# Performance work log

Measured on AMD Instinct MI355X. Metric: run time of the kernel, lower is better.

The kernel has to match this reference:

```python
import jax, jax.numpy as jnp
import numpy as np


def _conv1x1(W, x):
    # W: (out_c, in_c) from a 1x1 Conv2d (bias=False); x: (b, in_c, h, w)
    return jnp.einsum('oc,bchw->bohw', W, x)


def setup_inputs() -> dict:
    key = jax.random.key(0)
    ks = jax.random.split(key, 7)
    b, c, h, w = 4, 256, 64, 64
    inter = c // 2
    out_c = 256
    s = 0.02
    return {
        'A': jax.random.normal(ks[0], (b, c, h, w), dtype=jnp.float32),
        'B': jax.random.normal(ks[1], (b, c, h, w), dtype=jnp.float32),
        'W_phi': jax.random.normal(ks[2], (inter, c), dtype=jnp.float32) * s,
        'W_theta': jax.random.normal(ks[3], (inter, c), dtype=jnp.float32) * s,
        'W_g': jax.random.normal(ks[4], (inter, 2 * c), dtype=jnp.float32) * s,
        'W_AB': jax.random.normal(ks[5], (out_c, 2 * c), dtype=jnp.float32) * s,
        'W_mask': jax.random.normal(ks[6], (out_c, inter), dtype=jnp.float32) * s,
    }


def reference(A, B, W_phi, W_theta, W_g, W_AB, W_mask):
    b, c, h, w = A.shape
    inter = c // 2
    AB = jnp.concatenate([A, B], axis=1)  # (b, 2c, h, w)
    # NOTE: original torch code views (b, c/2, h*w) as (b, c, h*w/2) -> seq len N = h*w/2
    x_phi = _conv1x1(W_phi, A).reshape(b, c, -1)                       # (b, c, N)
    x_theta = _conv1x1(W_theta, B).reshape(b, c, -1).transpose(0, 2, 1)  # (b, N, c)
    x_g = _conv1x1(W_g, AB).reshape(b, c, -1).transpose(0, 2, 1)       # (b, N, c)
    scores = jnp.einsum('bnc,bcm->bnm', x_theta, x_phi)                # (b, N, N)
    attn = jax.nn.softmax(scores, axis=1)  # softmax over dim=1 as in torch code
    y = jnp.einsum('bnm,bmc->bnc', attn, x_g)                          # (b, N, c)
    y = y.transpose(0, 2, 1).reshape(b, inter, h, w)
    out = _conv1x1(W_mask, y) + _conv1x1(W_AB, AB)
    return out
```

## Files before the change

### kernel.cpp

```cpp
#include <hip/hip_runtime.h>
#include <hip/hip_bf16.h>

#define B_    4
#define C_    256
#define HW    4096
#define N_    2048
#define BSTR  524288

typedef unsigned short u16;
using f32x4 = __attribute__((ext_vector_type(4))) float;
using u32x4 = __attribute__((ext_vector_type(4))) unsigned int;

__device__ __forceinline__ float bf2f(u16 u) {
    return __uint_as_float(((unsigned)u) << 16);
}
__device__ __forceinline__ u16 f2bf(float f) {
    unsigned x = __float_as_uint(f);
    x += 0x7fff + ((x >> 16) & 1);
    return (u16)(x >> 16);
}

__device__ __forceinline__ void mfma_bf16(f32x4& acc, u32x4 a, u32x4 b) {
    asm volatile("v_mfma_f32_16x16x32_bf16 %0, %1, %2, %0"
                 : "+v"(acc) : "v"(a), "v"(b));
}
__device__ __forceinline__ void mfma_bf16_vsrc(f32x4& acc, u32x4 a, u32x4 b) {
    asm volatile("s_nop 1\n\tv_mfma_f32_16x16x32_bf16 %0, %1, %2, %0"
                 : "+v"(acc) : "v"(a), "v"(b));
}
__device__ __forceinline__ void mfma_fence(f32x4& x) {
    asm volatile("s_nop 7\n\ts_nop 7" : "+v"(x));
}

__global__ __launch_bounds__(256) void prep_w(
    const float* __restrict__ Wphi, const float* __restrict__ Wtheta,
    const float* __restrict__ Wg, const float* __restrict__ Wab,
    u16* __restrict__ Wt)
{
    const int row = blockIdx.x;
    const int t   = threadIdx.x;
    #pragma unroll
    for (int i = 0; i < 2; ++i) {
        const int col = i * 256 + t;
        float v;
        if (row < 128)      v = (col < 256)  ? Wphi[row * 256 + col] : 0.f;
        else if (row < 256) v = (col >= 256) ? Wtheta[(row - 128) * 256 + (col - 256)] : 0.f;
        else if (row < 384) v = Wg[(row - 256) * 512 + col];
        else                v = Wab[(row - 384) * 512 + col];
        Wt[row * 512 + col] = f2bf(v);
    }
}

__global__ __launch_bounds__(256) void prep_abt(
    const float* __restrict__ A, const float* __restrict__ Bx,
    u16* __restrict__ ABt)
{
    __shared__ u16 L[64][528];
    const int t = threadIdx.x, pb = blockIdx.x, b = blockIdx.y;
    const int p0 = pb * 64;
    const int pl = t & 63, cg = t >> 6;
    const float* Ab = A  + (size_t)b * C_ * HW;
    const float* Bb = Bx + (size_t)b * C_ * HW;

    for (int i = 0; i < 64; ++i) {
        const int c = cg + i * 4;
        L[pl][c]       = f2bf(Ab[c * HW + p0 + pl]);
        L[pl][256 + c] = f2bf(Bb[c * HW + p0 + pl]);
    }
    __syncthreads();
    u16* dst = ABt + ((size_t)b * 4096 + p0) * 512;
    #pragma unroll
    for (int i = 0; i < 16; ++i) {
        const int idx = i * 256 + t;
        const int row = idx >> 6, ch = idx & 63;
        *(uint4*)&dst[row * 512 + ch * 8] = *(const uint4*)&L[row][ch * 8];
    }
}

__global__ __launch_bounds__(256) void conv_gemm(
    const u16* __restrict__ Wt, const u16* __restrict__ ABt,
    u16* __restrict__ phit, u16* __restrict__ thetat,
    u16* __restrict__ g, float* __restrict__ out)
{
    __shared__ __align__(16) u16 shW[64 * 128];
    __shared__ __align__(16) u16 shAB[64 * 128];
    const int t = threadIdx.x, pb = blockIdx.x, nb = blockIdx.y, b = blockIdx.z;
    const int lane = t & 63, w = t >> 6, lo = lane & 15, hi = lane >> 4;
    const u16* Wb = Wt + nb * 64 * 512;
    const u16* Ab = ABt + ((size_t)b * 4096 + pb * 64) * 512;

    f32x4 acc[4];
    #pragma unroll
    for (int ot = 0; ot < 4; ++ot) acc[ot] = (f32x4){0.f, 0.f, 0.f, 0.f};

    for (int ks = 0; ks < 4; ++ks) {
        __syncthreads();
        #pragma unroll
        for (int i = 0; i < 4; ++i) {
            const int q = i * 256 + t;
            const int row = q >> 4, c16 = (q & 15) * 8;
            const int sw = (row & 7) << 3;
            *(uint4*)&shW[row * 128 + (c16 ^ sw)]  = *(const uint4*)&Wb[row * 512 + ks * 128 + c16];
            *(uint4*)&shAB[row * 128 + (c16 ^ sw)] = *(const uint4*)&Ab[row * 512 + ks * 128 + c16];
        }
        __syncthreads();
        u32x4 bfr[4];
        {
            const int row = w * 16 + lo, sw = (row & 7) << 3;
            #pragma unroll
            for (int kf = 0; kf < 4; ++kf)
                bfr[kf] = *(const u32x4*)&shAB[row * 128 + ((kf * 32 + hi * 8) ^ sw)];
        }
        #pragma unroll
        for (int ot = 0; ot < 4; ++ot) {
            const int row = ot * 16 + lo, sw = (row & 7) << 3;
            #pragma unroll
            for (int kf = 0; kf < 4; ++kf) {
                const u32x4 a = *(const u32x4*)&shW[row * 128 + ((kf * 32 + hi * 8) ^ sw)];
                mfma_bf16(acc[ot], a, bfr[kf]);
            }
        }
    }

    const int p_global = pb * 64 + w * 16 + lo;
    const int m = p_global & 2047, h = p_global >> 11;
    #pragma unroll
    for (int ot = 0; ot < 4; ++ot) {
        mfma_fence(acc[ot]);
        const int ob = nb * 64 + ot * 16 + hi * 4;
        if (nb < 2) {
            ushort4 v;
            v.x = f2bf(acc[ot][0]); v.y = f2bf(acc[ot][1]);
            v.z = f2bf(acc[ot][2]); v.w = f2bf(acc[ot][3]);
            *(ushort4*)&phit[(size_t)b * BSTR + m * 256 + h * 128 + ob] = v;
        } else if (nb < 4) {
            ushort4 v;
            v.x = f2bf(acc[ot][0]); v.y = f2bf(acc[ot][1]);
            v.z = f2bf(acc[ot][2]); v.w = f2bf(acc[ot][3]);
            *(ushort4*)&thetat[(size_t)b * BSTR + m * 256 + h * 128 + (ob - 128)] = v;
        } else if (nb < 6) {
            #pragma unroll
            for (int q = 0; q < 4; ++q)
                g[(size_t)b * BSTR + (ob - 256 + q) * HW + p_global] = f2bf(acc[ot][q]);
        } else {
            #pragma unroll
            for (int q = 0; q < 4; ++q)
                out[(size_t)b * C_ * HW + (size_t)(ob - 384 + q) * HW + p_global] = acc[ot][q];
        }
    }
}

__global__ __launch_bounds__(256) void passA_mfma(
    const u16* __restrict__ phit, const u16* __restrict__ thetat,
    float* __restrict__ rs)
{
    __shared__ __align__(16) u16 shP[64 * 256];
    __shared__ __align__(16) u16 shT[64 * 256];
    const int t = threadIdx.x, b = blockIdx.z, nq = blockIdx.y, mb = blockIdx.x;
    const u16* Pb = phit   + b * BSTR + mb * 64 * 256;
    const u16* Tb = thetat + b * BSTR + nq * 512 * 256;

    #pragma unroll
    for (int i = 0; i < 8; ++i) {
        const int q = i * 256 + t;
        const int row = q >> 5, c16 = (q & 31) * 8;
        const uint4 v = *(const uint4*)&Pb[row * 256 + c16];
        *(uint4*)&shP[row * 256 + (c16 ^ ((row & 7) << 3))] = v;
    }
    __syncthreads();

    const int lane = t & 63, w = t >> 6, lo = lane & 15, hi = lane >> 4;
    u32x4 afr[8];
    {
        const int row = w * 16 + lo;
        #pragma unroll
        for (int kb = 0; kb < 8; ++kb)
            afr[kb] = *(const u32x4*)&shP[row * 256 + ((kb * 32 + hi * 8) ^ ((row & 7) << 3))];
    }

    float rsacc[4] = {0.f, 0.f, 0.f, 0.f};
    for (int nt = 0; nt < 8; ++nt) {
        __syncthreads();
        #pragma unroll
        for (int i = 0; i < 8; ++i) {
            const int q = i * 256 + t;
            const int row = q >> 5, c16 = (q & 31) * 8;
            const uint4 v = *(const uint4*)&Tb[(nt * 64 + row) * 256 + c16];
            *(uint4*)&shT[row * 256 + (c16 ^ ((row & 7) << 3))] = v;
        }
        __syncthreads();
        #pragma unroll
        for (int ns = 0; ns < 4; ++ns) {
            f32x4 acc = {0.f, 0.f, 0.f, 0.f};
            const int row = ns * 16 + lo;
            #pragma unroll
            for (int kb = 0; kb < 8; ++kb) {
                const u32x4 bfr = *(const u32x4*)&shT[row * 256 + ((kb * 32 + hi * 8) ^ ((row & 7) << 3))];
                mfma_bf16(acc, afr[kb], bfr);
            }
            mfma_fence(acc);
            rsacc[0] += __expf(acc.x); rsacc[1] += __expf(acc.y);
            rsacc[2] += __expf(acc.z); rsacc[3] += __expf(acc.w);
        }
    }
    #pragma unroll
    for (int q = 0; q < 4; ++q) {
        float v = rsacc[q];
        v += __shfl_xor(v, 1); v += __shfl_xor(v, 2);
        v += __shfl_xor(v, 4); v += __shfl_xor(v, 8);
        rsacc[q] = v;
    }
    if (lo == 0) {
        const int m = mb * 64 + w * 16 + hi * 4;
        float* dst = rs + (nq * 4 + b) * N_ + m;
        dst[0] = rsacc[0]; dst[1] = rsacc[1]; dst[2] = rsacc[2]; dst[3] = rsacc[3];
    }
}

__global__ __launch_bounds__(256) void passB_mfma(
    const u16* __restrict__ phit, const u16* __restrict__ thetat,
    const u16* __restrict__ g, const float* __restrict__ rs,
    u16* __restrict__ Yt)
{
    __shared__ __align__(16) u16 shT[64 * 256];
    __shared__ __align__(16) u16 shPm[32 * 256];
    __shared__ __align__(16) u16 shG[64 * 32];
    __shared__ float shInv[32];

    const int t = threadIdx.x, b = blockIdx.z, ch = blockIdx.y, nb = blockIdx.x;
    const u16* Tb = thetat + b * BSTR + nb * 64 * 256;
    const u16* Pb = phit + b * BSTR;
    const u16* Gb = g + b * BSTR + ch * 64 * N_;
    const int lane = t & 63, w = t >> 6, lo = lane & 15, hi = lane >> 4;

    #pragma unroll
    for (int i = 0; i < 8; ++i) {
        const int q = i * 256 + t;
        const int row = q >> 5, c16 = (q & 31) * 8;
        const uint4 v = *(const uint4*)&Tb[row * 256 + c16];
        *(uint4*)&shT[row * 256 + (c16 ^ ((row & 7) << 3))] = v;
    }
    __syncthreads();
    u32x4 bfr[8];
    {
        const int row = w * 16 + lo;
        #pragma unroll
        for (int kb = 0; kb < 8; ++kb)
            bfr[kb] = *(const u32x4*)&shT[row * 256 + ((kb * 32 + hi * 8) ^ ((row & 7) << 3))];
    }

    f32x4 accY[4];
    #pragma unroll
    for (int ct = 0; ct < 4; ++ct) accY[ct] = (f32x4){0.f, 0.f, 0.f, 0.f};

    for (int mt = 0; mt < 64; ++mt) {
        __syncthreads();
        #pragma unroll
        for (int i = 0; i < 4; ++i) {
            const int q = i * 256 + t;
            const int row = q >> 5, c16 = (q & 31) * 8;
            const uint4 v = *(const uint4*)&Pb[(mt * 32 + row) * 256 + c16];
            *(uint4*)&shPm[row * 256 + (c16 ^ ((row & 7) << 3))] = v;
        }
        {
            const int row = t >> 2, qd = t & 3;
            const uint4 v = *(const uint4*)&Gb[row * N_ + mt * 32 + qd * 8];
            const int base = row * 32, m0 = qd * 8, sw = (row & 7) << 2;
            *(uint2*)&shG[base + ((m0    ) ^ sw)] = make_uint2(v.x, v.y);
            *(uint2*)&shG[base + ((m0 + 4) ^ sw)] = make_uint2(v.z, v.w);
        }
        if (t < 32) {
            const float* rp = rs + b * N_ + mt * 32 + t;
            shInv[t] = 1.0f / (rp[0] + rp[8192] + rp[16384] + rp[24576]);
        }
        __syncthreads();

        f32x4 s0 = {0.f, 0.f, 0.f, 0.f}, s1 = {0.f, 0.f, 0.f, 0.f};
        {
            const int row = lo;
            #pragma unroll
            for (int kb = 0; kb < 8; ++kb) {
                const u32x4 a = *(const u32x4*)&shPm[row * 256 + ((kb * 32 + hi * 8) ^ ((row & 7) << 3))];
                mfma_bf16(s0, a, bfr[kb]);
            }
        }
        {
            const int row = 16 + lo;
            #pragma unroll
            for (int kb = 0; kb < 8; ++kb) {
                const u32x4 a = *(const u32x4*)&shPm[row * 256 + ((kb * 32 + hi * 8) ^ ((row & 7) << 3))];
                mfma_bf16(s1, a, bfr[kb]);
            }
        }
        mfma_fence(s0); mfma_fence(s1);

        float p0[4], p1[4];
        #pragma unroll
        for (int q = 0; q < 4; ++q) {
            p0[q] = __expf(s0[q]) * shInv[hi * 4 + q];
            p1[q] = __expf(s1[q]) * shInv[16 + hi * 4 + q];
        }
        u32x4 pf;
        pf[0] = (unsigned)f2bf(p0[0]) | ((unsigned)f2bf(p0[1]) << 16);
        pf[1] = (unsigned)f2bf(p0[2]) | ((unsigned)f2bf(p0[3]) << 16);
        pf[2] = (unsigned)f2bf(p1[0]) | ((unsigned)f2bf(p1[1]) << 16);
        pf[3] = (unsigned)f2bf(p1[2]) | ((unsigned)f2bf(p1[3]) << 16);

        #pragma unroll
        for (int ct = 0; ct < 4; ++ct) {
            const int row = ct * 16 + lo;
            const int sw = (row & 7) << 2, m4 = hi * 4;
            const uint2 a0 = *(const uint2*)&shG[row * 32 + ((m4     ) ^ sw)];
            const uint2 a1 = *(const uint2*)&shG[row * 32 + ((16 + m4) ^ sw)];
            u32x4 gf; gf[0] = a0.x; gf[1] = a0.y; gf[2] = a1.x; gf[3] = a1.y;
            mfma_bf16_vsrc(accY[ct], gf, pf);
        }
    }

    u16* Yb = Yt + b * BSTR;
    #pragma unroll
    for (int ct = 0; ct < 4; ++ct) {
        mfma_fence(accY[ct]);
        const int crow = ch * 64 + ct * 16 + hi * 4;
        const int col  = nb * 64 + w * 16 + lo;
        #pragma unroll
        for (int q = 0; q < 4; ++q)
            Yb[(crow + q) * N_ + col] = f2bf(accY[ct][q]);
    }
}

__global__ __launch_bounds__(256) void mask_add_kernel(
    const u16* __restrict__ Yt, const float* __restrict__ Wm,
    float* __restrict__ out)
{
    const int p  = blockIdx.x * 256 + threadIdx.x;
    const int og = blockIdx.y;
    const int b  = blockIdx.z;
    const u16* Yb = Yt + b * BSTR;

    float acc[8] = {};
    for (int k = 0; k < 128; ++k) {
        const float y = bf2f(Yb[k * HW + p]);
        #pragma unroll
        for (int j = 0; j < 8; ++j)
            acc[j] = fmaf(Wm[(og * 8 + j) * 128 + k], y, acc[j]);
    }
    float* ob = out + (size_t)b * C_ * HW;
    #pragma unroll
    for (int j = 0; j < 8; ++j)
        ob[(og * 8 + j) * HW + p] += acc[j];
}

extern "C" void kernel_launch(void* const* d_in, const int* in_sizes, int n_in,
                              void* d_out, int out_size, void* d_ws, size_t ws_size,
                              hipStream_t stream)
{
    const float* A      = (const float*)d_in[0];
    const float* Bx     = (const float*)d_in[1];
    const float* Wphi   = (const float*)d_in[2];
    const float* Wtheta = (const float*)d_in[3];
    const float* Wg     = (const float*)d_in[4];
    const float* Wab    = (const float*)d_in[5];
    const float* Wmask  = (const float*)d_in[6];
    float* out = (float*)d_out;

    u16*   ABt    = (u16*)d_ws;
    u16*   Yt     = ABt;
    float* rs     = (float*)(ABt + 2097152);
    u16*   Wt     = ABt + 8388608;
    u16*   phit   = Wt + 327680;
    u16*   thetat = phit + 4 * BSTR / 2 * 2;
    u16*   g      = thetat + 2097152;

    prep_w<<<dim3(640), 256, 0, stream>>>(Wphi, Wtheta, Wg, Wab, Wt);

    prep_abt<<<dim3(64, 4), 256, 0, stream>>>(A, Bx, ABt);

    conv_gemm<<<dim3(64, 10, 4), 256, 0, stream>>>(
        Wt, ABt, phit, thetat, g, out);

    passA_mfma<<<dim3(32, 4, 4), 256, 0, stream>>>(phit, thetat, rs);

    passB_mfma<<<dim3(32, 4, 4), 256, 0, stream>>>(phit, thetat, g, rs, Yt);

    mask_add_kernel<<<dim3(16, 32, 4), 256, 0, stream>>>(Yt, Wmask, out);
}
```

Before: 276.1 us.

## Restructure passB to cover all channels per block with split-M partial sums

Each passB block now computes all 256 g-channels for its 64 query columns, so the QK^T score tile and its exp are computed once per block instead of once per channel chunk. The M range is split in two across blocks, and the two partial Y buffers are summed in mask_add. Softmax normalisation moves into a separate g_scale kernel that pre-scales g by the inverse column sums. Phi and g loads are software-prefetched into registers one iteration ahead. In exchange, each thread holds 16 accumulator tiles (higher register pressure), the grid has fewer blocks, and the extra kernel plus the doubled Y buffer add memory traffic.

```diff
diff --git a/kernel.cpp b/kernel.cpp
--- a/kernel.cpp
+++ b/kernel.cpp
@@ -217,20 +217,35 @@
     }
 }
 
+__global__ __launch_bounds__(256) void g_scale(
+    const float* __restrict__ rs, u16* __restrict__ g)
+{
+    const int t  = threadIdx.x;
+    const int mt = blockIdx.x;
+    const int cg = blockIdx.y;
+    const int b  = blockIdx.z;
+    const int m  = mt * 256 + t;
+    const float* rp = rs + b * N_ + m;
+    const float inv = 1.0f / (rp[0] + rp[8192] + rp[16384] + rp[24576]);
+    u16* gb = g + (size_t)b * BSTR + cg * 8 * N_ + m;
+    #pragma unroll
+    for (int j = 0; j < 8; ++j)
+        gb[j * N_] = f2bf(bf2f(gb[j * N_]) * inv);
+}
+
 __global__ __launch_bounds__(256) void passB_mfma(
     const u16* __restrict__ phit, const u16* __restrict__ thetat,
-    const u16* __restrict__ g, const float* __restrict__ rs,
-    u16* __restrict__ Yt)
-{
-    __shared__ __align__(16) u16 shT[64 * 256];
-    __shared__ __align__(16) u16 shPm[32 * 256];
-    __shared__ __align__(16) u16 shG[64 * 32];
-    __shared__ float shInv[32];
-
-    const int t = threadIdx.x, b = blockIdx.z, ch = blockIdx.y, nb = blockIdx.x;
+    const u16* __restrict__ g, u16* __restrict__ ytp)
+{
+    __shared__ __align__(16) u16 shBuf[64 * 256];
+    u16* shT  = shBuf;
+    u16* shPm = shBuf;
+    u16* shG  = shBuf + 32 * 256;
+
+    const int t = threadIdx.x, b = blockIdx.z, mh = blockIdx.y, nb = blockIdx.x;
     const u16* Tb = thetat + b * BSTR + nb * 64 * 256;
-    const u16* Pb = phit + b * BSTR;
-    const u16* Gb = g + b * BSTR + ch * 64 * N_;
+    const u16* Pb = phit   + b * BSTR + mh * 1024 * 256;
+    const u16* Gb = g      + b * BSTR;
     const int lane = t & 63, w = t >> 6, lo = lane & 15, hi = lane >> 4;
 
     #pragma unroll
@@ -248,31 +263,49 @@
         for (int kb = 0; kb < 8; ++kb)
             bfr[kb] = *(const u32x4*)&shT[row * 256 + ((kb * 32 + hi * 8) ^ ((row & 7) << 3))];
     }
-
-    f32x4 accY[4];
-    #pragma unroll
-    for (int ct = 0; ct < 4; ++ct) accY[ct] = (f32x4){0.f, 0.f, 0.f, 0.f};
-
-    for (int mt = 0; mt < 64; ++mt) {
+    __syncthreads();
+
+    f32x4 accY[16];
+    #pragma unroll
+    for (int ct = 0; ct < 16; ++ct) accY[ct] = (f32x4){0.f, 0.f, 0.f, 0.f};
+
+    uint4 vp[4], vg[4];
+    #pragma unroll
+    for (int i = 0; i < 4; ++i) {
+        const int q = i * 256 + t;
+        vp[i] = *(const uint4*)&Pb[(q >> 5) * 256 + (q & 31) * 8];
+    }
+    #pragma unroll
+    for (int qd = 0; qd < 4; ++qd)
+        vg[qd] = *(const uint4*)&Gb[(size_t)t * N_ + mh * 1024 + qd * 8];
+
+    for (int mt = 0; mt < 32; ++mt) {
         __syncthreads();
         #pragma unroll
         for (int i = 0; i < 4; ++i) {
             const int q = i * 256 + t;
             const int row = q >> 5, c16 = (q & 31) * 8;
-            const uint4 v = *(const uint4*)&Pb[(mt * 32 + row) * 256 + c16];
-            *(uint4*)&shPm[row * 256 + (c16 ^ ((row & 7) << 3))] = v;
+            *(uint4*)&shPm[row * 256 + (c16 ^ ((row & 7) << 3))] = vp[i];
         }
         {
-            const int row = t >> 2, qd = t & 3;
-            const uint4 v = *(const uint4*)&Gb[row * N_ + mt * 32 + qd * 8];
-            const int base = row * 32, m0 = qd * 8, sw = (row & 7) << 2;
-            *(uint2*)&shG[base + ((m0    ) ^ sw)] = make_uint2(v.x, v.y);
-            *(uint2*)&shG[base + ((m0 + 4) ^ sw)] = make_uint2(v.z, v.w);
-        }
-        if (t < 32) {
-            const float* rp = rs + b * N_ + mt * 32 + t;
-            shInv[t] = 1.0f / (rp[0] + rp[8192] + rp[16384] + rp[24576]);
-        }
+            const int sw = (t & 7) << 2, base = t * 32;
+            #pragma unroll
+            for (int qd = 0; qd < 4; ++qd) {
+                const int m0 = qd * 8;
+                *(uint2*)&shG[base + ((m0    ) ^ sw)] = make_uint2(vg[qd].x, vg[qd].y);
+                *(uint2*)&shG[base + ((m0 + 4) ^ sw)] = make_uint2(vg[qd].z, vg[qd].w);
+            }
+        }
+        const int mtn = (mt < 31) ? mt + 1 : 31;
+        uint4 vp2[4], vg2[4];
+        #pragma unroll
+        for (int i = 0; i < 4; ++i) {
+            const int q = i * 256 + t;
+            vp2[i] = *(const uint4*)&Pb[(mtn * 32 + (q >> 5)) * 256 + (q & 31) * 8];
+        }
+        #pragma unroll
+        for (int qd = 0; qd < 4; ++qd)
+            vg2[qd] = *(const uint4*)&Gb[(size_t)t * N_ + mh * 1024 + mtn * 32 + qd * 8];
         __syncthreads();
 
         f32x4 s0 = {0.f, 0.f, 0.f, 0.f}, s1 = {0.f, 0.f, 0.f, 0.f};
@@ -297,8 +330,8 @@
         float p0[4], p1[4];
         #pragma unroll
         for (int q = 0; q < 4; ++q) {
-            p0[q] = __expf(s0[q]) * shInv[hi * 4 + q];
-            p1[q] = __expf(s1[q]) * shInv[16 + hi * 4 + q];
+            p0[q] = __expf(s0[q]);
+            p1[q] = __expf(s1[q]);
         }
         u32x4 pf;
         pf[0] = (unsigned)f2bf(p0[0]) | ((unsigned)f2bf(p0[1]) << 16);
@@ -307,7 +340,7 @@
         pf[3] = (unsigned)f2bf(p1[2]) | ((unsigned)f2bf(p1[3]) << 16);
 
         #pragma unroll
-        for (int ct = 0; ct < 4; ++ct) {
+        for (int ct = 0; ct < 16; ++ct) {
             const int row = ct * 16 + lo;
             const int sw = (row & 7) << 2, m4 = hi * 4;
             const uint2 a0 = *(const uint2*)&shG[row * 32 + ((m4     ) ^ sw)];
@@ -315,14 +348,19 @@
             u32x4 gf; gf[0] = a0.x; gf[1] = a0.y; gf[2] = a1.x; gf[3] = a1.y;
             mfma_bf16_vsrc(accY[ct], gf, pf);
         }
-    }
-
-    u16* Yb = Yt + b * BSTR;
-    #pragma unroll
-    for (int ct = 0; ct < 4; ++ct) {
+
+        #pragma unroll
+        for (int i = 0; i < 4; ++i) vp[i] = vp2[i];
+        #pragma unroll
+        for (int qd = 0; qd < 4; ++qd) vg[qd] = vg2[qd];
+    }
+
+    u16* Yb = ytp + ((size_t)mh * B_ + b) * BSTR;
+    const int col = nb * 64 + w * 16 + lo;
+    #pragma unroll
+    for (int ct = 0; ct < 16; ++ct) {
         mfma_fence(accY[ct]);
-        const int crow = ch * 64 + ct * 16 + hi * 4;
-        const int col  = nb * 64 + w * 16 + lo;
+        const int crow = ct * 16 + hi * 4;
         #pragma unroll
         for (int q = 0; q < 4; ++q)
             Yb[(crow + q) * N_ + col] = f2bf(accY[ct][q]);
@@ -330,17 +368,18 @@
 }
 
 __global__ __launch_bounds__(256) void mask_add_kernel(
-    const u16* __restrict__ Yt, const float* __restrict__ Wm,
+    const u16* __restrict__ ytp, const float* __restrict__ Wm,
     float* __restrict__ out)
 {
     const int p  = blockIdx.x * 256 + threadIdx.x;
     const int og = blockIdx.y;
     const int b  = blockIdx.z;
-    const u16* Yb = Yt + b * BSTR;
+    const u16* Y0 = ytp + (size_t)b * BSTR;
+    const u16* Y1 = ytp + ((size_t)B_ + b) * BSTR;
 
     float acc[8] = {};
     for (int k = 0; k < 128; ++k) {
-        const float y = bf2f(Yb[k * HW + p]);
+        const float y = bf2f(Y0[k * HW + p]) + bf2f(Y1[k * HW + p]);
         #pragma unroll
         for (int j = 0; j < 8; ++j)
             acc[j] = fmaf(Wm[(og * 8 + j) * 128 + k], y, acc[j]);
@@ -365,11 +404,11 @@
     float* out = (float*)d_out;
 
     u16*   ABt    = (u16*)d_ws;
-    u16*   Yt     = ABt;
-    float* rs     = (float*)(ABt + 2097152);
+    u16*   ytp    = ABt;
+    float* rs     = (float*)(ABt + 4194304);
     u16*   Wt     = ABt + 8388608;
     u16*   phit   = Wt + 327680;
-    u16*   thetat = phit + 4 * BSTR / 2 * 2;
+    u16*   thetat = phit + 2097152;
     u16*   g      = thetat + 2097152;
 
     prep_w<<<dim3(640), 256, 0, stream>>>(Wphi, Wtheta, Wg, Wab, Wt);
@@ -381,7 +420,9 @@
 
     passA_mfma<<<dim3(32, 4, 4), 256, 0, stream>>>(phit, thetat, rs);
 
-    passB_mfma<<<dim3(32, 4, 4), 256, 0, stream>>>(phit, thetat, g, rs, Yt);
-
-    mask_add_kernel<<<dim3(16, 32, 4), 256, 0, stream>>>(Yt, Wmask, out);
-}
+    g_scale<<<dim3(8, 32, 4), 256, 0, stream>>>(rs, g);
+
+    passB_mfma<<<dim3(32, 2, 4), 256, 0, stream>>>(phit, thetat, g, ytp);
+
+    mask_add_kernel<<<dim3(16, 32, 4), 256, 0, stream>>>(ytp, Wmask, out);
+}
```

Measured after the change: 284.6 us. +3.1%, slower.
